# Kernel tuning notes

Hardware: AMD Instinct MI355X
Metric: run time of the kernel (lower is better)

Reference implementation:

```python
import jax, jax.numpy as jnp
import numpy as np

N = 50000
E = 800000
IN_F = 128
HID_F = 128
OUT_F = 128
BN_EPS = 1e-5


def make_quaternion_mul(kernel):
    # kernel: [d_in//4, d_out]; returns hamilton: [d_in, d_out]
    r, i, j, k = jnp.split(kernel, 4, axis=1)
    r2 = jnp.concatenate([r, -i, -j, -k], axis=0)
    i2 = jnp.concatenate([i, r, -k, j], axis=0)
    j2 = jnp.concatenate([j, k, r, -i], axis=0)
    k2 = jnp.concatenate([k, -j, i, r], axis=0)
    return jnp.concatenate([r2, i2, j2, k2], axis=1)


def setup_inputs() -> dict:
    key = jax.random.key(0)
    k1, k2, k3, k4, k5, k6 = jax.random.split(key, 6)
    stdv = np.sqrt(6.0 / (IN_F // 4 + HID_F)).astype(np.float32)
    inputs = {
        "input": jax.random.normal(k1, (N, IN_F), dtype=jnp.float32),
        "adj_row": jnp.sort(jax.random.randint(k2, (E,), 0, N, dtype=jnp.int32)),
        "adj_col": jax.random.randint(k3, (E,), 0, N, dtype=jnp.int32),
        "adj_val": jax.random.uniform(k4, (E,), dtype=jnp.float32),
        "weight1": jax.random.uniform(k5, (IN_F // 4, HID_F), minval=-stdv, maxval=stdv, dtype=jnp.float32),
        "weight2": jax.random.uniform(k6, (HID_F // 4, OUT_F), minval=-stdv, maxval=stdv, dtype=jnp.float32),
        "gamma": jnp.ones((OUT_F,), dtype=jnp.float32),
        "beta": jnp.zeros((OUT_F,), dtype=jnp.float32),
    }
    return inputs


def reference(input, adj_row, adj_col, adj_val, weight1, weight2, gamma, beta):
    hamilton1 = make_quaternion_mul(weight1)  # [IN_F, HID_F]
    hamilton2 = make_quaternion_mul(weight2)  # [HID_F, OUT_F]
    out1 = jnp.tanh(input @ hamilton1)        # [N, HID_F]
    out2 = out1 @ hamilton2                   # [N, OUT_F]
    # sparse adj (COO) x dense: out[i] = sum_e val[e] * out2[col[e]] for row[e]==i
    gathered = adj_val[:, None] * out2[adj_col]  # [E, OUT_F]
    agg = jax.ops.segment_sum(gathered, adj_row, num_segments=N)  # [N, OUT_F]
    # BatchNorm1d (training mode): per-feature stats over nodes, biased var
    mean = jnp.mean(agg, axis=0)
    var = jnp.var(agg, axis=0)
    return gamma * (agg - mean) * jax.lax.rsqrt(var + BN_EPS) + beta
```

## Files before the change

kernel.cpp:

```cpp
#include <hip/hip_runtime.h>
#include <cstddef>
#include <cstdint>

#define F 128
#define LDK 136
#define AGG_BLOCKS 2048
#define MID_BLOCKS 64

typedef __attribute__((ext_vector_type(8))) short short8;
typedef __attribute__((ext_vector_type(4))) float f32x4;

__device__ __forceinline__ short f2bf(float f) {
  uint32_t u = __float_as_uint(f);
  uint32_t r = u + 0x7FFFu + ((u >> 16) & 1u);
  return (short)(r >> 16);
}
__device__ __forceinline__ float bf2f(short h) {
  return __uint_as_float(((uint32_t)(uint16_t)h) << 16);
}

__global__ __launch_bounds__(256) void setup_kernel(
    const float* __restrict__ w1, const float* __restrict__ w2,
    short* __restrict__ Hpk, const int* __restrict__ adj_row,
    const int* __restrict__ adj_col, const float* __restrict__ adj_val,
    int* __restrict__ rowptr, uint2* __restrict__ cv, int E, int N) {
  if (blockIdx.x < 16) {
    int idx = blockIdx.x * 256 + threadIdx.x;
    int m = idx >> 11;
    int kt = (idx >> 9) & 3;
    int ct = (idx >> 6) & 7;
    int l = idx & 63;
    int col = ct * 16 + (l & 15);
    const float* w = m ? w2 : w1;
    short hi[8], lo[8];
#pragma unroll
    for (int j = 0; j < 8; ++j) {
      int row = kt * 32 + (l >> 4) * 8 + j;
      int rb = row >> 5, cb = col >> 5;
      int neg = (0x284E >> (cb * 4 + rb)) & 1;
      float v = w[(row & 31) * 128 + (rb ^ cb) * 32 + (col & 31)];
      v = neg ? -v : v;
      short h = f2bf(v);
      hi[j] = h;
      lo[j] = f2bf(v - bf2f(h));
    }
    size_t b0 = ((((size_t)m * 2 + 0) * 4 + kt) * 8 + ct) * 64 + l;
    size_t b1 = ((((size_t)m * 2 + 1) * 4 + kt) * 8 + ct) * 64 + l;
    *(short8*)&Hpk[b0 * 8] = *(short8*)hi;
    *(short8*)&Hpk[b1 * 8] = *(short8*)lo;
  } else {
    int e = (blockIdx.x - 16) * 256 + threadIdx.x;
    if (e >= E) return;
    cv[e] = make_uint2((uint32_t)adj_col[e], __float_as_uint(adj_val[e]));
    int r = adj_row[e];
    int rprev = (e == 0) ? -1 : adj_row[e - 1];
    for (int q = rprev + 1; q <= r; ++q) rowptr[q] = e;
    if (e == E - 1) {
      for (int q = r + 1; q <= N; ++q) rowptr[q] = E;
    }
  }
}

__global__ __launch_bounds__(256) void gemm_mfma(
    const float* __restrict__ input, const short* __restrict__ Hpk,
    short* __restrict__ out2b, int N) {
  __shared__ short Hs[16384];
  __shared__ short lds[4][16 * LDK];
  const int t = threadIdx.x;
  const int w = t >> 6, l = t & 63;
  const int lr = l & 15, lg = l >> 4;
  const int grow0 = blockIdx.x * 64 + w * 16;
  short* hid = &lds[w][0];

#define STAGE_HALF(m, P)                                             \
  {                                                                  \
    const int base = ((m) * 8 + 2 * (P)) * 512;                      \
    _Pragma("unroll") for (int i = 0; i < 8; ++i) {                  \
      int idx = i * 256 + t;                                         \
      int src = idx + base + (idx >> 10) * 1024;                     \
      *(short8*)&Hs[idx * 8] = *(const short8*)&Hpk[src * 8];        \
    }                                                                \
  }

#define GEMM_HALF(afrag, P)                                                          \
  {                                                                                  \
    _Pragma("unroll") for (int ktl = 0; ktl < 2; ++ktl) {                            \
      _Pragma("unroll") for (int ct = 0; ct < 8; ++ct) {                             \
        short8 bh = *(const short8*)&Hs[((ktl * 8 + ct) * 64 + l) * 8];              \
        short8 bl = *(const short8*)&Hs[(((2 + ktl) * 8 + ct) * 64 + l) * 8];        \
        acc[ct] = __builtin_amdgcn_mfma_f32_16x16x32_bf16(afrag[2 * (P) + ktl], bl,  \
                                                          acc[ct], 0, 0, 0);         \
        acc[ct] = __builtin_amdgcn_mfma_f32_16x16x32_bf16(afrag[2 * (P) + ktl], bh,  \
                                                          acc[ct], 0, 0, 0);         \
      }                                                                              \
    }                                                                                \
  }

  short8 a1h[4];
  {
    int arow = grow0 + lr;
    if (arow >= N) arow = N - 1;
    const float* xr = &input[(size_t)arow * F];
#pragma unroll
    for (int kt = 0; kt < 4; ++kt) {
      float xv[8];
      *(float4*)&xv[0] = *(const float4*)&xr[kt * 32 + lg * 8];
      *(float4*)&xv[4] = *(const float4*)&xr[kt * 32 + lg * 8 + 4];
#pragma unroll
      for (int j = 0; j < 8; ++j) ((short*)&a1h[kt])[j] = f2bf(xv[j]);
    }
  }

  f32x4 acc[8];
#pragma unroll
  for (int ct = 0; ct < 8; ++ct) acc[ct] = (f32x4){0.f, 0.f, 0.f, 0.f};

  STAGE_HALF(0, 0)
  __syncthreads();
  GEMM_HALF(a1h, 0)
  __syncthreads();
  STAGE_HALF(0, 1)
  __syncthreads();
  GEMM_HALF(a1h, 1)

#pragma unroll
  for (int ct = 0; ct < 8; ++ct)
#pragma unroll
    for (int r = 0; r < 4; ++r)
      hid[(lg * 4 + r) * LDK + ct * 16 + lr] = f2bf(tanhf(acc[ct][r]));

  short8 a2h[4];
#pragma unroll
  for (int kt = 0; kt < 4; ++kt)
    a2h[kt] = *(short8*)&hid[lr * LDK + kt * 32 + lg * 8];

#pragma unroll
  for (int ct = 0; ct < 8; ++ct) acc[ct] = (f32x4){0.f, 0.f, 0.f, 0.f};

  __syncthreads();
  STAGE_HALF(1, 0)
  __syncthreads();
  GEMM_HALF(a2h, 0)
  __syncthreads();
  STAGE_HALF(1, 1)
  __syncthreads();
  GEMM_HALF(a2h, 1)

#pragma unroll
  for (int ct = 0; ct < 8; ++ct)
#pragma unroll
    for (int r = 0; r < 4; ++r)
      hid[(lg * 4 + r) * LDK + ct * 16 + lr] = f2bf(acc[ct][r]);
#pragma unroll
  for (int i = 0; i < 4; ++i) {
    int chunk = i * 64 + l;
    int row = chunk >> 4, pos = chunk & 15;
    int grow = grow0 + row;
    if (grow < N)
      *(short8*)&out2b[(size_t)grow * F + pos * 8] = *(short8*)&hid[row * LDK + pos * 8];
  }
#undef STAGE_HALF
#undef GEMM_HALF
}

__global__ __launch_bounds__(256) void agg_rows7(
    const uint32_t* __restrict__ out2u,
    const int* __restrict__ rowptr, const uint2* __restrict__ cv,
    float* __restrict__ agg, float* __restrict__ partials, int N) {
  const int t = threadIdx.x;
  const int w = t >> 6, lane = t & 63;
  const int sub = lane >> 4;
  const int fl4 = (lane & 15) * 4;
  const int wid = blockIdx.x * 4 + w;
  const int nw = gridDim.x * 4;
  float ssum[8], ssq[8];
#pragma unroll
  for (int j = 0; j < 8; ++j) { ssum[j] = 0.f; ssq[j] = 0.f; }

  int pr = wid;
  bool active = pr * 2 < N;
  int sA = 0, eAe = 0, eBe = 0;
  if (active) {
    sA = rowptr[pr * 2];
    eAe = rowptr[pr * 2 + 1];
    eBe = (pr * 2 + 1 < N) ? rowptr[pr * 2 + 2] : eAe;
  }
  while (active) {
    const int prn = pr + nw;
    const bool actn = prn * 2 < N;
    int sAn = 0, eAen = 0, eBen = 0;
    if (actn) {
      sAn = rowptr[prn * 2];
      eAen = rowptr[prn * 2 + 1];
      eBen = (prn * 2 + 1 < N) ? rowptr[prn * 2 + 2] : eAen;
    }
    const int rowA = pr * 2;
    const bool hasB = rowA + 1 < N;
    const int sB = eAe;

    float accA[8], accB[8];
#pragma unroll
    for (int j = 0; j < 8; ++j) { accA[j] = 0.f; accB[j] = 0.f; }

    int eA = sA, eB = sB;
    while (eA < eAe || eB < eBe) {
      float vA[4], vB[4];
      uint32_t cA[4], cB[4];
#pragma unroll
      for (int q = 0; q < 4; ++q) {
        int ee = eA + q * 4 + sub;
        bool val = ee < eAe;
        int idx = val ? ee : (eAe - 1);
        idx = idx < 0 ? 0 : idx;
        uint2 p = cv[idx];
        cA[q] = p.x;
        vA[q] = val ? __uint_as_float(p.y) : 0.f;
      }
#pragma unroll
      for (int q = 0; q < 4; ++q) {
        int ee = eB + q * 4 + sub;
        bool val = ee < eBe;
        int idx = val ? ee : (eBe - 1);
        idx = idx < 0 ? 0 : idx;
        uint2 p = cv[idx];
        cB[q] = p.x;
        vB[q] = val ? __uint_as_float(p.y) : 0.f;
      }
      uint4 uA[4], uB[4];
#pragma unroll
      for (int q = 0; q < 4; ++q)
        uA[q] = *(const uint4*)&out2u[(size_t)(cA[q] * 64u + fl4)];
#pragma unroll
      for (int q = 0; q < 4; ++q)
        uB[q] = *(const uint4*)&out2u[(size_t)(cB[q] * 64u + fl4)];
#pragma unroll
      for (int q = 0; q < 4; ++q) {
#pragma unroll
        for (int k = 0; k < 4; ++k) {
          uint32_t ua = ((const uint32_t*)&uA[q])[k];
          uint32_t ub = ((const uint32_t*)&uB[q])[k];
          accA[2 * k]     = fmaf(vA[q], __uint_as_float(ua << 16), accA[2 * k]);
          accA[2 * k + 1] = fmaf(vA[q], __uint_as_float(ua & 0xFFFF0000u), accA[2 * k + 1]);
          accB[2 * k]     = fmaf(vB[q], __uint_as_float(ub << 16), accB[2 * k]);
          accB[2 * k + 1] = fmaf(vB[q], __uint_as_float(ub & 0xFFFF0000u), accB[2 * k + 1]);
        }
      }
      eA += 16;
      eB += 16;
    }
#pragma unroll
    for (int j = 0; j < 8; ++j) {
      accA[j] += __shfl_xor(accA[j], 16, 64);
      accA[j] += __shfl_xor(accA[j], 32, 64);
      accB[j] += __shfl_xor(accB[j], 16, 64);
      accB[j] += __shfl_xor(accB[j], 32, 64);
    }
    if (sub == 0) {
      *(float4*)&agg[(size_t)rowA * F + fl4 * 2] = make_float4(accA[0], accA[1], accA[2], accA[3]);
      *(float4*)&agg[(size_t)rowA * F + fl4 * 2 + 4] = make_float4(accA[4], accA[5], accA[6], accA[7]);
#pragma unroll
      for (int j = 0; j < 8; ++j) {
        ssum[j] += accA[j];
        ssq[j] = fmaf(accA[j], accA[j], ssq[j]);
      }
      if (hasB) {
        *(float4*)&agg[(size_t)(rowA + 1) * F + fl4 * 2] = make_float4(accB[0], accB[1], accB[2], accB[3]);
        *(float4*)&agg[(size_t)(rowA + 1) * F + fl4 * 2 + 4] = make_float4(accB[4], accB[5], accB[6], accB[7]);
#pragma unroll
        for (int j = 0; j < 8; ++j) {
          ssum[j] += accB[j];
          ssq[j] = fmaf(accB[j], accB[j], ssq[j]);
        }
      }
    }
    pr = prn;
    sA = sAn; eAe = eAen; eBe = eBen;
    active = actn;
  }

  __shared__ float ls[4][128];
  __shared__ float lq[4][128];
  if (sub == 0) {
#pragma unroll
    for (int j = 0; j < 8; ++j) {
      ls[w][fl4 * 2 + j] = ssum[j];
      lq[w][fl4 * 2 + j] = ssq[j];
    }
  }
  __syncthreads();
  if (t < 128) {
    float S = ls[0][t] + ls[1][t] + ls[2][t] + ls[3][t];
    float Q = lq[0][t] + lq[1][t] + lq[2][t] + lq[3][t];
    float* dst = &partials[(size_t)blockIdx.x * 256];
    dst[t] = S;
    dst[128 + t] = Q;
  }
}

__global__ __launch_bounds__(256) void mid_reduce(
    const float* __restrict__ partials, float* __restrict__ mid, int nb) {
  const int k = blockIdx.x, t = threadIdx.x;
  const int per = nb / MID_BLOCKS;
  float s = 0.f;
#pragma unroll 4
  for (int i = 0; i < per; ++i)
    s += partials[(size_t)(k * per + i) * 256 + t];
  mid[(size_t)k * 256 + t] = s;
}

__global__ __launch_bounds__(256) void finalize_stats3(
    const float* __restrict__ mid, const float* __restrict__ gamma,
    const float* __restrict__ beta, float* __restrict__ ss, float invN) {
  const int t = threadIdx.x;
  float s = 0.f;
#pragma unroll 8
  for (int b = 0; b < MID_BLOCKS; ++b) s += mid[(size_t)b * 256 + t];
  __shared__ float tot[256];
  tot[t] = s;
  __syncthreads();
  if (t < 128) {
    float mean = tot[t] * invN;
    float var = tot[128 + t] * invN - mean * mean;
    float inv = rsqrtf(var + 1e-5f);
    float sc = gamma[t] * inv;
    ss[t] = sc;
    ss[128 + t] = beta[t] - mean * sc;
  }
}

__global__ __launch_bounds__(256) void bn_apply(
    float* __restrict__ out, const float* __restrict__ ss, int total4) {
  int idx = blockIdx.x * 256 + threadIdx.x;
  if (idx >= total4) return;
  int f4 = (idx & 31) * 4;
  float4 v = *(float4*)&out[(size_t)idx * 4];
  float4 sc = *(const float4*)&ss[f4];
  float4 sh = *(const float4*)&ss[128 + f4];
  v.x = fmaf(v.x, sc.x, sh.x);
  v.y = fmaf(v.y, sc.y, sh.y);
  v.z = fmaf(v.z, sc.z, sh.z);
  v.w = fmaf(v.w, sc.w, sh.w);
  *(float4*)&out[(size_t)idx * 4] = v;
}

extern "C" void kernel_launch(void* const* d_in, const int* in_sizes, int n_in,
                              void* d_out, int out_size, void* d_ws, size_t ws_size,
                              hipStream_t stream) {
  (void)n_in; (void)out_size; (void)ws_size;
  const float* input  = (const float*)d_in[0];
  const int*  adj_row = (const int*)d_in[1];
  const int*  adj_col = (const int*)d_in[2];
  const float* adj_val = (const float*)d_in[3];
  const float* w1 = (const float*)d_in[4];
  const float* w2 = (const float*)d_in[5];
  const float* gamma = (const float*)d_in[6];
  const float* beta  = (const float*)d_in[7];
  const int N = in_sizes[0] / F;
  const int E = in_sizes[1];

  char* ws = (char*)d_ws;
  short* Hpk = (short*)(ws);
  float* ss = (float*)(ws + 131072);
  float* partials = (float*)(ws + 132096);
  float* mid = (float*)(ws + 2229248);
  int* rowptr = (int*)(ws + 2294784);
  uint2* cv = (uint2*)(ws + 2499584);
  size_t cv_bytes = ((size_t)E * 8 + 511) & ~(size_t)511;
  short* out2b = (short*)(ws + 2499584 + cv_bytes);
  float* agg = (float*)d_out;

  setup_kernel<<<16 + (E + 255) / 256, 256, 0, stream>>>(
      w1, w2, Hpk, adj_row, adj_col, adj_val, rowptr, cv, E, N);
  gemm_mfma<<<(N + 63) / 64, 256, 0, stream>>>(input, Hpk, out2b, N);
  agg_rows7<<<AGG_BLOCKS, 256, 0, stream>>>(
      (const uint32_t*)out2b, rowptr, cv, agg, partials, N);
  mid_reduce<<<MID_BLOCKS, 256, 0, stream>>>(partials, mid, AGG_BLOCKS);
  finalize_stats3<<<1, 256, 0, stream>>>(mid, gamma, beta, ss, 1.0f / (float)N);
  bn_apply<<<(N * 32 + 255) / 256, 256, 0, stream>>>(agg, ss, N * 32);
}
```

Baseline: 83.06 us.

## Move COO preprocessing into GEMM launch and fuse stat reductions via last-block counter

Splits weight packing into its own small kernel and folds the edge-list conversion (rowptr/cv construction) into the GEMM launch as extra blocks, so edge preprocessing runs concurrently with the MFMA GEMM instead of before it. The mid-level and final BatchNorm stat reductions are merged into one kernel using an atomic counter so the last finishing block computes scale/shift, removing a launch. The counter is reset inside the aggregation kernel. The cost is a larger GEMM grid with heavy LDS declared in every block, including the preprocessing-only blocks, which may reduce their occupancy.

```diff
diff --git a/kernel.cpp b/kernel.cpp
--- a/kernel.cpp
+++ b/kernel.cpp
@@ -19,37 +19,43 @@
   return __uint_as_float(((uint32_t)(uint16_t)h) << 16);
 }
 
-__global__ __launch_bounds__(256) void setup_kernel(
+__global__ __launch_bounds__(256) void hpk_pack(
     const float* __restrict__ w1, const float* __restrict__ w2,
-    short* __restrict__ Hpk, const int* __restrict__ adj_row,
+    short* __restrict__ Hpk) {
+  int idx = blockIdx.x * 256 + threadIdx.x;
+  int m = idx >> 11;
+  int kt = (idx >> 9) & 3;
+  int ct = (idx >> 6) & 7;
+  int l = idx & 63;
+  int col = ct * 16 + (l & 15);
+  const float* w = m ? w2 : w1;
+  short hi[8], lo[8];
+#pragma unroll
+  for (int j = 0; j < 8; ++j) {
+    int row = kt * 32 + (l >> 4) * 8 + j;
+    int rb = row >> 5, cb = col >> 5;
+    int neg = (0x284E >> (cb * 4 + rb)) & 1;
+    float v = w[(row & 31) * 128 + (rb ^ cb) * 32 + (col & 31)];
+    v = neg ? -v : v;
+    short h = f2bf(v);
+    hi[j] = h;
+    lo[j] = f2bf(v - bf2f(h));
+  }
+  size_t b0 = ((((size_t)m * 2 + 0) * 4 + kt) * 8 + ct) * 64 + l;
+  size_t b1 = ((((size_t)m * 2 + 1) * 4 + kt) * 8 + ct) * 64 + l;
+  *(short8*)&Hpk[b0 * 8] = *(short8*)hi;
+  *(short8*)&Hpk[b1 * 8] = *(short8*)lo;
+}
+
+__global__ __launch_bounds__(256) void gemm_plus(
+    const float* __restrict__ input, const short* __restrict__ Hpk,
+    short* __restrict__ out2b, const int* __restrict__ adj_row,
     const int* __restrict__ adj_col, const float* __restrict__ adj_val,
-    int* __restrict__ rowptr, uint2* __restrict__ cv, int E, int N) {
-  if (blockIdx.x < 16) {
-    int idx = blockIdx.x * 256 + threadIdx.x;
-    int m = idx >> 11;
-    int kt = (idx >> 9) & 3;
-    int ct = (idx >> 6) & 7;
-    int l = idx & 63;
-    int col = ct * 16 + (l & 15);
-    const float* w = m ? w2 : w1;
-    short hi[8], lo[8];
-#pragma unroll
-    for (int j = 0; j < 8; ++j) {
-      int row = kt * 32 + (l >> 4) * 8 + j;
-      int rb = row >> 5, cb = col >> 5;
-      int neg = (0x284E >> (cb * 4 + rb)) & 1;
-      float v = w[(row & 31) * 128 + (rb ^ cb) * 32 + (col & 31)];
-      v = neg ? -v : v;
-      short h = f2bf(v);
-      hi[j] = h;
-      lo[j] = f2bf(v - bf2f(h));
-    }
-    size_t b0 = ((((size_t)m * 2 + 0) * 4 + kt) * 8 + ct) * 64 + l;
-    size_t b1 = ((((size_t)m * 2 + 1) * 4 + kt) * 8 + ct) * 64 + l;
-    *(short8*)&Hpk[b0 * 8] = *(short8*)hi;
-    *(short8*)&Hpk[b1 * 8] = *(short8*)lo;
-  } else {
-    int e = (blockIdx.x - 16) * 256 + threadIdx.x;
+    int* __restrict__ rowptr, uint2* __restrict__ cv, int E, int N, int gb) {
+  __shared__ short Hs[16384];
+  __shared__ short lds[4][16 * LDK];
+  if (blockIdx.x >= gb) {
+    int e = (blockIdx.x - gb) * 256 + threadIdx.x;
     if (e >= E) return;
     cv[e] = make_uint2((uint32_t)adj_col[e], __float_as_uint(adj_val[e]));
     int r = adj_row[e];
@@ -58,14 +64,8 @@
     if (e == E - 1) {
       for (int q = r + 1; q <= N; ++q) rowptr[q] = E;
     }
-  }
-}
-
-__global__ __launch_bounds__(256) void gemm_mfma(
-    const float* __restrict__ input, const short* __restrict__ Hpk,
-    short* __restrict__ out2b, int N) {
-  __shared__ short Hs[16384];
-  __shared__ short lds[4][16 * LDK];
+    return;
+  }
   const int t = threadIdx.x;
   const int w = t >> 6, l = t & 63;
   const int lr = l & 15, lg = l >> 4;
@@ -164,15 +164,16 @@
 }
 
 __global__ __launch_bounds__(256) void agg_rows7(
-    const uint32_t* __restrict__ out2u,
-    const int* __restrict__ rowptr, const uint2* __restrict__ cv,
-    float* __restrict__ agg, float* __restrict__ partials, int N) {
+    const uint32_t* __restrict__ out2u, const int* __restrict__ rowptr,
+    const uint2* __restrict__ cv, float* __restrict__ agg,
+    float* __restrict__ partials, uint32_t* __restrict__ ctr, int N) {
   const int t = threadIdx.x;
   const int w = t >> 6, lane = t & 63;
   const int sub = lane >> 4;
   const int fl4 = (lane & 15) * 4;
   const int wid = blockIdx.x * 4 + w;
   const int nw = gridDim.x * 4;
+  if (blockIdx.x == 0 && t == 0) *ctr = 0u;
   float ssum[8], ssq[8];
 #pragma unroll
   for (int j = 0; j < 8; ++j) { ssum[j] = 0.f; ssq[j] = 0.f; }
@@ -297,8 +298,10 @@
   }
 }
 
-__global__ __launch_bounds__(256) void mid_reduce(
-    const float* __restrict__ partials, float* __restrict__ mid, int nb) {
+__global__ __launch_bounds__(256) void midfin(
+    const float* __restrict__ partials, float* __restrict__ mid,
+    const float* __restrict__ gamma, const float* __restrict__ beta,
+    float* __restrict__ ss, uint32_t* __restrict__ ctr, float invN, int nb) {
   const int k = blockIdx.x, t = threadIdx.x;
   const int per = nb / MID_BLOCKS;
   float s = 0.f;
@@ -306,17 +309,18 @@
   for (int i = 0; i < per; ++i)
     s += partials[(size_t)(k * per + i) * 256 + t];
   mid[(size_t)k * 256 + t] = s;
-}
-
-__global__ __launch_bounds__(256) void finalize_stats3(
-    const float* __restrict__ mid, const float* __restrict__ gamma,
-    const float* __restrict__ beta, float* __restrict__ ss, float invN) {
-  const int t = threadIdx.x;
-  float s = 0.f;
+  __threadfence();
+  __syncthreads();
+  __shared__ bool last;
+  if (t == 0) last = (atomicAdd(ctr, 1u) == MID_BLOCKS - 1);
+  __syncthreads();
+  if (!last) return;
+  __threadfence();
+  float s2 = 0.f;
 #pragma unroll 8
-  for (int b = 0; b < MID_BLOCKS; ++b) s += mid[(size_t)b * 256 + t];
+  for (int b = 0; b < MID_BLOCKS; ++b) s2 += mid[(size_t)b * 256 + t];
   __shared__ float tot[256];
-  tot[t] = s;
+  tot[t] = s2;
   __syncthreads();
   if (t < 128) {
     float mean = tot[t] * invN;
@@ -361,20 +365,22 @@
   char* ws = (char*)d_ws;
   short* Hpk = (short*)(ws);
   float* ss = (float*)(ws + 131072);
-  float* partials = (float*)(ws + 132096);
-  float* mid = (float*)(ws + 2229248);
-  int* rowptr = (int*)(ws + 2294784);
-  uint2* cv = (uint2*)(ws + 2499584);
+  uint32_t* ctr = (uint32_t*)(ws + 132096);
+  float* partials = (float*)(ws + 132608);
+  float* mid = (float*)(ws + 2229760);
+  int* rowptr = (int*)(ws + 2295296);
+  uint2* cv = (uint2*)(ws + 2500096);
   size_t cv_bytes = ((size_t)E * 8 + 511) & ~(size_t)511;
-  short* out2b = (short*)(ws + 2499584 + cv_bytes);
+  short* out2b = (short*)(ws + 2500096 + cv_bytes);
   float* agg = (float*)d_out;
 
-  setup_kernel<<<16 + (E + 255) / 256, 256, 0, stream>>>(
-      w1, w2, Hpk, adj_row, adj_col, adj_val, rowptr, cv, E, N);
-  gemm_mfma<<<(N + 63) / 64, 256, 0, stream>>>(input, Hpk, out2b, N);
+  const int gb = (N + 63) / 64;
+  hpk_pack<<<16, 256, 0, stream>>>(w1, w2, Hpk);
+  gemm_plus<<<gb + (E + 255) / 256, 256, 0, stream>>>(
+      input, Hpk, out2b, adj_row, adj_col, adj_val, rowptr, cv, E, N, gb);
   agg_rows7<<<AGG_BLOCKS, 256, 0, stream>>>(
-      (const uint32_t*)out2b, rowptr, cv, agg, partials, N);
-  mid_reduce<<<MID_BLOCKS, 256, 0, stream>>>(partials, mid, AGG_BLOCKS);
-  finalize_stats3<<<1, 256, 0, stream>>>(mid, gamma, beta, ss, 1.0f / (float)N);
+      (const uint32_t*)out2b, rowptr, cv, agg, partials, ctr, N);
+  midfin<<<MID_BLOCKS, 256, 0, stream>>>(partials, mid, gamma, beta, ss, ctr,
+                                         1.0f / (float)N, AGG_BLOCKS);
   bn_apply<<<(N * 32 + 255) / 256, 256, 0, stream>>>(agg, ss, N * 32);
 }
```

Result: slower. 86.07 us (+3.6%).
